# Performance work log

Hardware: AMD Instinct MI355X
Metric: run time of the kernel (lower is better)

Reference implementation:

```python
import jax, jax.numpy as jnp
import numpy as np

D = 256      # d_model
H = 8        # n_heads
L = 4        # n_levels
P = 4        # n_points
DFF = 1024   # d_ffn
DH = D // H  # head dim
SPATIAL = np.array([[100, 100], [50, 50], [25, 25], [13, 13]], dtype=np.int64)  # (H_l, W_l)
LV = int((SPATIAL[:, 0] * SPATIAL[:, 1]).sum())  # 13294 flattened memory tokens


def layer_norm(x, w, b, eps=1e-5):
    m = jnp.mean(x, -1, keepdims=True)
    v = jnp.mean((x - m) ** 2, -1, keepdims=True)
    return (x - m) * jax.lax.rsqrt(v + eps) * w + b


def setup_inputs() -> dict:
    key = jax.random.key(0)
    ks = jax.random.split(key, 16)
    nq, bs = 900, 8

    def w(k, shape, s=0.02):
        return jax.random.normal(k, shape, dtype=jnp.float32) * s

    return {
        "tgt": jax.random.normal(ks[0], (nq, bs, D), jnp.float32),
        "tgt_query_pos": jax.random.normal(ks[1], (nq, bs, D), jnp.float32),
        "tgt_reference_points": jax.random.uniform(ks[2], (nq, bs, L, 2), jnp.float32),
        "memory": jax.random.normal(ks[3], (LV, bs, D), jnp.float32),
        "sa_Wqkv": w(ks[4], (3 * D, D)), "sa_bqkv": jnp.zeros((3 * D,), jnp.float32),
        "sa_Wo": w(ks[5], (D, D)), "sa_bo": jnp.zeros((D,), jnp.float32),
        "ln1_w": jnp.ones((D,), jnp.float32), "ln1_b": jnp.zeros((D,), jnp.float32),
        "ln2_w": jnp.ones((D,), jnp.float32), "ln2_b": jnp.zeros((D,), jnp.float32),
        "ln3_w": jnp.ones((D,), jnp.float32), "ln3_b": jnp.zeros((D,), jnp.float32),
        "ca_Woff": w(ks[6], (H * L * P * 2, D)), "ca_boff": w(ks[7], (H * L * P * 2,), 0.5),
        "ca_Wattn": w(ks[8], (H * L * P, D)), "ca_battn": jnp.zeros((H * L * P,), jnp.float32),
        "ca_Wval": w(ks[9], (D, D)), "ca_bval": jnp.zeros((D,), jnp.float32),
        "ca_Wout": w(ks[10], (D, D)), "ca_bout": jnp.zeros((D,), jnp.float32),
        "ffn_W1": w(ks[11], (DFF, D)), "ffn_b1": jnp.zeros((DFF,), jnp.float32),
        "ffn_W2": w(ks[12], (D, DFF)), "ffn_b2": jnp.zeros((D,), jnp.float32),
        "memory_key_padding_mask": jnp.zeros((bs, LV), jnp.bool_),
        "memory_spatial_shapes": jnp.asarray(SPATIAL),
    }


def msdeform_attn(query, ref, value, mask, shapes_np,
                  Woff, boff, Wattn, battn, Wval, bval, Wout, bout):
    # query: [bs,nq,D], ref: [bs,nq,L,2], value: [bs,lv,D], mask: [bs,lv]
    bs, nq, _ = query.shape
    lv = value.shape[1]
    v = value @ Wval.T + bval
    v = jnp.where(mask[:, :, None], 0.0, v)
    v = v.reshape(bs, lv, H, DH).transpose(0, 2, 1, 3)  # [bs,H,lv,DH]
    off = (query @ Woff.T + boff).reshape(bs, nq, H, L, P, 2)
    aw = jax.nn.softmax((query @ Wattn.T + battn).reshape(bs, nq, H, L * P), -1)
    aw = aw.reshape(bs, nq, H, L, P)
    # offset normalizer is [W_l, H_l]
    norm = jnp.asarray(shapes_np[:, ::-1].copy(), jnp.float32)  # [L,2]
    loc = ref[:, :, None, :, None, :] + off / norm[None, None, None, :, None, :]
    out = jnp.zeros((bs, nq, H, DH), jnp.float32)
    start = 0
    for l in range(L):
        Hl, Wl = int(shapes_np[l, 0]), int(shapes_np[l, 1])
        vf = v[:, :, start:start + Hl * Wl]  # [bs,H,Hl*Wl,DH]
        start += Hl * Wl
        # grid_sample(align_corners=False) pixel coords
        x = loc[:, :, :, l, :, 0] * Wl - 0.5  # [bs,nq,H,P]
        y = loc[:, :, :, l, :, 1] * Hl - 0.5
        x0 = jnp.floor(x); y0 = jnp.floor(y)
        fx = x - x0; fy = y - y0
        x0i = x0.astype(jnp.int32); y0i = y0.astype(jnp.int32)

        def gather(yi, xi):
            valid = ((xi >= 0) & (xi < Wl) & (yi >= 0) & (yi < Hl)).astype(jnp.float32)
            idx = jnp.clip(yi, 0, Hl - 1) * Wl + jnp.clip(xi, 0, Wl - 1)
            idx_t = idx.transpose(0, 2, 1, 3).reshape(bs, H, nq * P, 1)
            g = jnp.take_along_axis(vf, idx_t, axis=2)  # [bs,H,nq*P,DH]
            return g * valid.transpose(0, 2, 1, 3).reshape(bs, H, nq * P, 1)

        def wgt(w):
            return w.transpose(0, 2, 1, 3).reshape(bs, H, nq * P, 1)

        samp = (gather(y0i, x0i) * wgt((1 - fx) * (1 - fy))
                + gather(y0i, x0i + 1) * wgt(fx * (1 - fy))
                + gather(y0i + 1, x0i) * wgt((1 - fx) * fy)
                + gather(y0i + 1, x0i + 1) * wgt(fx * fy))
        samp = samp.reshape(bs, H, nq, P, DH)
        out = out + jnp.einsum('bhqpd,bqhp->bqhd', samp, aw[:, :, :, l])
    return out.reshape(bs, nq, D) @ Wout.T + bout


def reference(tgt, tgt_query_pos, tgt_reference_points, memory,
              sa_Wqkv, sa_bqkv, sa_Wo, sa_bo,
              ln1_w, ln1_b, ln2_w, ln2_b, ln3_w, ln3_b,
              ca_Woff, ca_boff, ca_Wattn, ca_battn, ca_Wval, ca_bval, ca_Wout, ca_bout,
              ffn_W1, ffn_b1, ffn_W2, ffn_b2,
              memory_key_padding_mask, memory_spatial_shapes):
    shapes_np = np.asarray(memory_spatial_shapes)  # static per trace
    nq, bs, _ = tgt.shape
    # --- self attention (post-LN, residual) ---
    q = tgt + tgt_query_pos
    qp = (q @ sa_Wqkv[:D].T + sa_bqkv[:D]).reshape(nq, bs, H, DH)
    kp = (q @ sa_Wqkv[D:2 * D].T + sa_bqkv[D:2 * D]).reshape(nq, bs, H, DH)
    vp = (tgt @ sa_Wqkv[2 * D:].T + sa_bqkv[2 * D:]).reshape(nq, bs, H, DH)
    scores = jnp.einsum('qbhd,kbhd->bhqk', qp, kp) * (1.0 / float(np.sqrt(DH)))
    attn = jax.nn.softmax(scores, -1)
    o = jnp.einsum('bhqk,kbhd->qbhd', attn, vp).reshape(nq, bs, D) @ sa_Wo.T + sa_bo
    tgt = layer_norm(tgt + o, ln2_w, ln2_b)
    # --- multi-scale deformable cross attention ---
    query = (tgt + tgt_query_pos).transpose(1, 0, 2)      # [bs,nq,D]
    ref = tgt_reference_points.transpose(1, 0, 2, 3)      # [bs,nq,L,2]
    val = memory.transpose(1, 0, 2)                       # [bs,lv,D]
    ca = msdeform_attn(query, ref, val, memory_key_padding_mask, shapes_np,
                       ca_Woff, ca_boff, ca_Wattn, ca_battn,
                       ca_Wval, ca_bval, ca_Wout, ca_bout).transpose(1, 0, 2)
    tgt = layer_norm(tgt + ca, ln1_w, ln1_b)
    # --- FFN ---
    t2 = jax.nn.relu(tgt @ ffn_W1.T + ffn_b1) @ ffn_W2.T + ffn_b2
    return layer_norm(tgt + t2, ln3_w, ln3_b)
```

## Files before the change

### kernel.cpp

```cpp
#include <hip/hip_runtime.h>
#include <hip/hip_bf16.h>

#define NQ   900
#define BSZ  8
#define DM   256
#define NH   8
#define DHD  32
#define DFF_ 1024
#define LVTOT 13294
#define NTOK (NQ*BSZ)
#define MVAL (LVTOT*BSZ)

typedef __attribute__((ext_vector_type(8))) short bf16x8;
typedef __attribute__((ext_vector_type(4))) short bf16x4;
typedef __attribute__((ext_vector_type(4))) float f32x4;
typedef unsigned int u32;

__device__ __forceinline__ unsigned short f2bf(float x) {
  union { __hip_bfloat16 h; unsigned short u; } cv;
  cv.h = __float2bfloat16(x);
  return cv.u;
}
__device__ __forceinline__ float bf2f(unsigned short u) {
  union { __hip_bfloat16 h; unsigned short u; } cv;
  cv.u = u;
  return __bfloat162float(cv.h);
}

__device__ __forceinline__ void gl_lds16(const void* gsrc, void* ldst) {
  __builtin_amdgcn_global_load_lds(
      (const __attribute__((address_space(1))) u32*)gsrc,
      (__attribute__((address_space(3))) u32*)ldst, 16, 0, 0);
}

__global__ __launch_bounds__(256) void cast_kernel(const float* __restrict__ src,
                                                   unsigned short* __restrict__ dst, int n8) {
  int i = blockIdx.x * 256 + threadIdx.x;
  if (i >= n8) return;
  float4 a = ((const float4*)src)[i * 2];
  float4 b = ((const float4*)src)[i * 2 + 1];
  bf16x8 v;
  v[0] = (short)f2bf(a.x); v[1] = (short)f2bf(a.y);
  v[2] = (short)f2bf(a.z); v[3] = (short)f2bf(a.w);
  v[4] = (short)f2bf(b.x); v[5] = (short)f2bf(b.y);
  v[6] = (short)f2bf(b.z); v[7] = (short)f2bf(b.w);
  *(bf16x8*)(dst + (long)i * 8) = v;
}

__global__ __launch_bounds__(256) void addcast_kernel(const float* __restrict__ a,
                                                      const float* __restrict__ b,
                                                      unsigned short* __restrict__ o, int n8) {
  int i = blockIdx.x * 256 + threadIdx.x;
  if (i >= n8) return;
  float4 a0 = ((const float4*)a)[i * 2], a1 = ((const float4*)a)[i * 2 + 1];
  float4 b0 = ((const float4*)b)[i * 2], b1 = ((const float4*)b)[i * 2 + 1];
  bf16x8 v;
  v[0] = (short)f2bf(a0.x + b0.x); v[1] = (short)f2bf(a0.y + b0.y);
  v[2] = (short)f2bf(a0.z + b0.z); v[3] = (short)f2bf(a0.w + b0.w);
  v[4] = (short)f2bf(a1.x + b1.x); v[5] = (short)f2bf(a1.y + b1.y);
  v[6] = (short)f2bf(a1.z + b1.z); v[7] = (short)f2bf(a1.w + b1.w);
  *(bf16x8*)(o + (long)i * 8) = v;
}

__global__ __launch_bounds__(256) void cast_weights_kernel(
    const float* p0, const float* p1, const float* p2, const float* p3,
    const float* p4, const float* p5, const float* p6, const float* p7,
    unsigned short* dst) {
  long i8 = ((long)blockIdx.x * 256 + threadIdx.x) * 8;
  if (i8 >= 1015808) return;
  const float* src; long off;
  if      (i8 < 196608) { src = p0; off = i8; }
  else if (i8 < 262144) { src = p1; off = i8 - 196608; }
  else if (i8 < 327680) { src = p2; off = i8 - 262144; }
  else if (i8 < 393216) { src = p3; off = i8 - 327680; }
  else if (i8 < 425984) { src = p4; off = i8 - 393216; }
  else if (i8 < 491520) { src = p5; off = i8 - 425984; }
  else if (i8 < 753664) { src = p6; off = i8 - 491520; }
  else                  { src = p7; off = i8 - 753664; }
  float4 a = *(const float4*)(src + off);
  float4 b = *(const float4*)(src + off + 4);
  bf16x8 v;
  v[0] = (short)f2bf(a.x); v[1] = (short)f2bf(a.y);
  v[2] = (short)f2bf(a.z); v[3] = (short)f2bf(a.w);
  v[4] = (short)f2bf(b.x); v[5] = (short)f2bf(b.y);
  v[6] = (short)f2bf(b.z); v[7] = (short)f2bf(b.w);
  *(bf16x8*)(dst + i8) = v;
}

template <int AF32, int OUT_BF16, int RELU>
__global__ __launch_bounds__(256) void gemm_mfma_kernel(
    const void* __restrict__ Araw, const unsigned short* __restrict__ W,
    const float* __restrict__ bias, void* __restrict__ C,
    int M, int K, int ldc) {
  __shared__ unsigned short As[128 * 32];
  __shared__ unsigned short Bs[128 * 32];
  int tid = threadIdx.x;
  int l = tid & 63, w = tid >> 6;
  int lr = l & 15, lg = l >> 4;
  int wr = w >> 1, wc = w & 1;
  int n0 = blockIdx.x * 128, m0 = blockIdx.y * 128;

  f32x4 acc[4][4];
#pragma unroll
  for (int m = 0; m < 4; m++)
#pragma unroll
    for (int n = 0; n < 4; n++) acc[m][n] = (f32x4){0.f, 0.f, 0.f, 0.f};

  int srow = (l >> 2);
  int scol = (l & 3) * 8;

  for (int k0 = 0; k0 < K; k0 += 32) {
    if (k0) __syncthreads();
    if (AF32) {
      const float* Af = (const float*)Araw;
      int row = tid >> 1, c16 = (tid & 1) * 16;
      int arow = m0 + row; if (arow >= M) arow = M - 1;
      const float* ap = Af + (long)arow * K + k0 + c16;
      float4 f0 = *(const float4*)(ap + 0);
      float4 f1 = *(const float4*)(ap + 4);
      float4 f2 = *(const float4*)(ap + 8);
      float4 f3 = *(const float4*)(ap + 12);
      bf16x8 v0, v1;
      v0[0] = (short)f2bf(f0.x); v0[1] = (short)f2bf(f0.y);
      v0[2] = (short)f2bf(f0.z); v0[3] = (short)f2bf(f0.w);
      v0[4] = (short)f2bf(f1.x); v0[5] = (short)f2bf(f1.y);
      v0[6] = (short)f2bf(f1.z); v0[7] = (short)f2bf(f1.w);
      v1[0] = (short)f2bf(f2.x); v1[1] = (short)f2bf(f2.y);
      v1[2] = (short)f2bf(f2.z); v1[3] = (short)f2bf(f2.w);
      v1[4] = (short)f2bf(f3.x); v1[5] = (short)f2bf(f3.y);
      v1[6] = (short)f2bf(f3.z); v1[7] = (short)f2bf(f3.w);
      *(bf16x8*)&As[row * 32 + c16] = v0;
      *(bf16x8*)&As[row * 32 + c16 + 8] = v1;
      int browi = w * 16 + srow;
#pragma unroll
      for (int c = 0; c < 2; c++) {
        int row2 = c * 64 + browi;
        gl_lds16(W + (long)(n0 + row2) * K + k0 + scol, (char*)Bs + row2 * 64 + scol * 2);
      }
    } else {
      const unsigned short* A = (const unsigned short*)Araw;
#pragma unroll
      for (int c = 0; c < 2; c++) {
        int row = c * 64 + w * 16 + srow;
        if (m0 + c * 64 + w * 16 < M)
          gl_lds16(A + (long)(m0 + row) * K + k0 + scol, (char*)As + row * 64 + scol * 2);
        gl_lds16(W + (long)(n0 + row) * K + k0 + scol, (char*)Bs + row * 64 + scol * 2);
      }
    }
    __syncthreads();
    bf16x8 af[4], bf[4];
#pragma unroll
    for (int m = 0; m < 4; m++)
      af[m] = *(const bf16x8*)&As[(wr * 64 + m * 16 + lr) * 32 + lg * 8];
#pragma unroll
    for (int n = 0; n < 4; n++)
      bf[n] = *(const bf16x8*)&Bs[(wc * 64 + n * 16 + lr) * 32 + lg * 8];
#pragma unroll
    for (int m = 0; m < 4; m++)
#pragma unroll
      for (int n = 0; n < 4; n++)
        acc[m][n] = __builtin_amdgcn_mfma_f32_16x16x32_bf16(af[m], bf[n], acc[m][n], 0, 0, 0);
  }

  float bv[4];
#pragma unroll
  for (int ni = 0; ni < 4; ni++) bv[ni] = bias[n0 + wc * 64 + ni * 16 + lr];
#pragma unroll
  for (int mi = 0; mi < 4; mi++) {
#pragma unroll
    for (int r = 0; r < 4; r++) {
      int row = m0 + wr * 64 + mi * 16 + lg * 4 + r;
      if (row < M) {
#pragma unroll
        for (int ni = 0; ni < 4; ni++) {
          int col = n0 + wc * 64 + ni * 16 + lr;
          float v = acc[mi][ni][r] + bv[ni];
          if (RELU) v = fmaxf(v, 0.f);
          if (OUT_BF16) ((unsigned short*)C)[(long)row * ldc + col] = f2bf(v);
          else          ((float*)C)[(long)row * ldc + col] = v;
        }
      }
    }
  }
}

__global__ __launch_bounds__(256) void attn_mfma_kernel(const unsigned short* __restrict__ qkv,
                                                        unsigned short* __restrict__ out) {
  __shared__ unsigned short Vt[32][72];
  __shared__ unsigned short Ps[4][16][72];
  int tid = threadIdx.x;
  int l = tid & 63, w = tid >> 6;
  int lr = l & 15, lg = l >> 4;
  int q0 = blockIdx.x * 64;
  int h = blockIdx.y & 7, b = blockIdx.y >> 3;
  const float scale = 0.17677669529663687f;

  int qrow = q0 + w * 16 + lr;
  int qclamp = qrow < 899 ? qrow : 899;
  bf16x8 qf = *(const bf16x8*)(qkv + ((long)qclamp * 8 + b) * 768 + h * 32 + lg * 8);

  f32x4 o_acc[2];
  o_acc[0] = (f32x4){0.f, 0.f, 0.f, 0.f};
  o_acc[1] = (f32x4){0.f, 0.f, 0.f, 0.f};
  float m_run[4] = {-1e30f, -1e30f, -1e30f, -1e30f};
  float l_run[4] = {0.f, 0.f, 0.f, 0.f};

  for (int k0 = 0; k0 < NQ; k0 += 64) {
    __syncthreads();
    {
      int key = tid >> 2, dg = tid & 3;
      int kk = k0 + key; if (kk > 899) kk = 899;
      bf16x8 vv = *(const bf16x8*)(qkv + ((long)kk * 8 + b) * 768 + 512 + h * 32 + dg * 8);
#pragma unroll
      for (int j = 0; j < 8; j++) Vt[dg * 8 + j][key] = (unsigned short)vv[j];
    }
    f32x4 sg[4];
#pragma unroll
    for (int ng = 0; ng < 4; ng++) {
      int key = k0 + ng * 16 + lr; int kc = key < 899 ? key : 899;
      bf16x8 kf = *(const bf16x8*)(qkv + ((long)kc * 8 + b) * 768 + 256 + h * 32 + lg * 8);
      sg[ng] = __builtin_amdgcn_mfma_f32_16x16x32_bf16(qf, kf, (f32x4){0.f, 0.f, 0.f, 0.f}, 0, 0, 0);
    }
    float sv[4][4];
#pragma unroll
    for (int ng = 0; ng < 4; ng++) {
      bool bad = (k0 + ng * 16 + lr) >= NQ;
#pragma unroll
      for (int r = 0; r < 4; r++) sv[ng][r] = bad ? -1e30f : sg[ng][r] * scale;
    }
    float p[4][4];
#pragma unroll
    for (int r = 0; r < 4; r++) {
      float rmax = fmaxf(fmaxf(sv[0][r], sv[1][r]), fmaxf(sv[2][r], sv[3][r]));
#pragma unroll
      for (int mk = 8; mk; mk >>= 1) rmax = fmaxf(rmax, __shfl_xor(rmax, mk));
      float mnew = fmaxf(m_run[r], rmax);
      float fs = __expf(m_run[r] - mnew);
      m_run[r] = mnew;
      float ps = 0.f;
#pragma unroll
      for (int ng = 0; ng < 4; ng++) { p[ng][r] = __expf(sv[ng][r] - mnew); ps += p[ng][r]; }
#pragma unroll
      for (int mk = 8; mk; mk >>= 1) ps += __shfl_xor(ps, mk);
      l_run[r] = l_run[r] * fs + ps;
      o_acc[0][r] *= fs;
      o_acc[1][r] *= fs;
    }
#pragma unroll
    for (int ng = 0; ng < 4; ng++)
#pragma unroll
      for (int r = 0; r < 4; r++)
        Ps[w][lg * 4 + r][lr + ng * 16] = f2bf(p[ng][r]);
    __syncthreads();
#pragma unroll
    for (int ks = 0; ks < 2; ks++) {
      bf16x8 pf = *(const bf16x8*)&Ps[w][lr][ks * 32 + lg * 8];
#pragma unroll
      for (int ni = 0; ni < 2; ni++) {
        bf16x8 vf = *(const bf16x8*)&Vt[ni * 16 + lr][ks * 32 + lg * 8];
        o_acc[ni] = __builtin_amdgcn_mfma_f32_16x16x32_bf16(pf, vf, o_acc[ni], 0, 0, 0);
      }
    }
  }
#pragma unroll
  for (int r = 0; r < 4; r++) {
    int orow = q0 + w * 16 + lg * 4 + r;
    if (orow < NQ) {
      float inv = 1.f / l_run[r];
      unsigned short* op = out + ((long)orow * 8 + b) * 256 + h * 32 + lr;
      op[0]  = f2bf(o_acc[0][r] * inv);
      op[16] = f2bf(o_acc[1][r] * inv);
    }
  }
}

__device__ __forceinline__ void fetch4_acc(const unsigned short* __restrict__ vtmp, int lo, int W,
                                           int yi, int xi, int b, int col0, float wgt,
                                           float& a0, float& a1, float& a2, float& a3) {
  bool valid = (xi >= 0) & (xi < W) & (yi >= 0) & (yi < W);
  if (!valid) return;
  const unsigned short* p = vtmp + ((long)((lo + yi * W + xi) * BSZ + b)) * 256 + col0;
  bf16x4 r = *(const bf16x4*)p;
  a0 += wgt * bf2f((unsigned short)r[0]);
  a1 += wgt * bf2f((unsigned short)r[1]);
  a2 += wgt * bf2f((unsigned short)r[2]);
  a3 += wgt * bf2f((unsigned short)r[3]);
}

__global__ __launch_bounds__(256) void sampler_kernel(const unsigned short* __restrict__ vtmp,
                                                      const float* __restrict__ off,
                                                      const float* __restrict__ logits,
                                                      const float* __restrict__ ref,
                                                      unsigned short* __restrict__ samp) {
  __shared__ float s_off[4][256];
  __shared__ float s_aw[4][128];
  __shared__ float s_ref[4][8];
  int tid = threadIdx.x;
  int t0 = blockIdx.x * 4;
#pragma unroll
  for (int k = 0; k < 4; k++) s_off[k][tid] = off[(long)(t0 + k) * 256 + tid];
  if (tid < 128) {
#pragma unroll
    for (int k = 0; k < 4; k++) s_aw[k][tid] = logits[(long)(t0 + k) * 128 + tid];
  }
  if (tid < 32) s_ref[tid >> 3][tid & 7] = ref[(long)(t0 + (tid >> 3)) * 8 + (tid & 7)];
  __syncthreads();
  if (tid < 32) {
    int k = tid >> 3, hh = tid & 7;
    float* p = &s_aw[k][hh * 16];
    float m = -1e30f;
#pragma unroll
    for (int j = 0; j < 16; j++) m = fmaxf(m, p[j]);
    float s = 0.f;
#pragma unroll
    for (int j = 0; j < 16; j++) { p[j] = __expf(p[j] - m); s += p[j]; }
    float inv = 1.f / s;
#pragma unroll
    for (int j = 0; j < 16; j++) p[j] *= inv;
  }
  __syncthreads();
  int w = tid >> 6, l = tid & 63;
  int t = t0 + w;
  int h = l >> 3, col0 = h * 32 + (l & 7) * 4;
  int b = t & 7;
  const int Wls[4]  = {100, 50, 25, 13};
  const int lofs[4] = {0, 10000, 12500, 13125};
  float a0 = 0.f, a1 = 0.f, a2 = 0.f, a3 = 0.f;
#pragma unroll
  for (int lvl = 0; lvl < 4; lvl++) {
    int W = Wls[lvl];
    float Wf = (float)W;
    int lo = lofs[lvl];
    float rx = s_ref[w][lvl * 2 + 0], ry = s_ref[w][lvl * 2 + 1];
#pragma unroll
    for (int p = 0; p < 4; p++) {
      float ox = s_off[w][((h * 4 + lvl) * 4 + p) * 2 + 0];
      float oy = s_off[w][((h * 4 + lvl) * 4 + p) * 2 + 1];
      float x = rx * Wf + ox - 0.5f;
      float y = ry * Wf + oy - 0.5f;
      float x0f = floorf(x), y0f = floorf(y);
      float fx = x - x0f, fy = y - y0f;
      int x0 = (int)x0f, y0 = (int)y0f;
      float aa = s_aw[w][h * 16 + lvl * 4 + p];
      float w00 = aa * (1.f - fx) * (1.f - fy);
      float w01 = aa * fx * (1.f - fy);
      float w10 = aa * (1.f - fx) * fy;
      float w11 = aa * fx * fy;
      fetch4_acc(vtmp, lo, W, y0,     x0,     b, col0, w00, a0, a1, a2, a3);
      fetch4_acc(vtmp, lo, W, y0,     x0 + 1, b, col0, w01, a0, a1, a2, a3);
      fetch4_acc(vtmp, lo, W, y0 + 1, x0,     b, col0, w10, a0, a1, a2, a3);
      fetch4_acc(vtmp, lo, W, y0 + 1, x0 + 1, b, col0, w11, a0, a1, a2, a3);
    }
  }
  bf16x4 o;
  o[0] = (short)f2bf(a0); o[1] = (short)f2bf(a1);
  o[2] = (short)f2bf(a2); o[3] = (short)f2bf(a3);
  *(bf16x4*)(samp + (long)t * 256 + col0) = o;
}

__global__ __launch_bounds__(256) void ln_kernel(const float* __restrict__ x,
                                                 const float* __restrict__ res,
                                                 const float* __restrict__ w,
                                                 const float* __restrict__ bvec,
                                                 float* __restrict__ out,
                                                 unsigned short* __restrict__ out_bf,
                                                 const float* __restrict__ pos,
                                                 unsigned short* __restrict__ pos_bf,
                                                 int rows) {
  int wv = threadIdx.x >> 6, lane = threadIdx.x & 63;
  int row = blockIdx.x * 4 + wv;
  if (row >= rows) return;
  float4 xv = *(const float4*)(x + (long)row * 256 + lane * 4);
  float4 rv = *(const float4*)(res + (long)row * 256 + lane * 4);
  float v0 = xv.x + rv.x, v1 = xv.y + rv.y, v2 = xv.z + rv.z, v3 = xv.w + rv.w;
  float s = v0 + v1 + v2 + v3;
#pragma unroll
  for (int o = 32; o; o >>= 1) s += __shfl_xor(s, o);
  float mean = s * (1.f / 256.f);
  float d0 = v0 - mean, d1 = v1 - mean, d2 = v2 - mean, d3 = v3 - mean;
  float q = d0 * d0 + d1 * d1 + d2 * d2 + d3 * d3;
#pragma unroll
  for (int o = 32; o; o >>= 1) q += __shfl_xor(q, o);
  float rstd = rsqrtf(q * (1.f / 256.f) + 1e-5f);
  float4 wv4 = *(const float4*)(w + lane * 4);
  float4 bv4 = *(const float4*)(bvec + lane * 4);
  float o0 = d0 * rstd * wv4.x + bv4.x;
  float o1 = d1 * rstd * wv4.y + bv4.y;
  float o2 = d2 * rstd * wv4.z + bv4.z;
  float o3 = d3 * rstd * wv4.w + bv4.w;
  *(float4*)(out + (long)row * 256 + lane * 4) = make_float4(o0, o1, o2, o3);
  if (out_bf) {
    unsigned short* p = out_bf + (long)row * 256 + lane * 4;
    p[0] = f2bf(o0); p[1] = f2bf(o1); p[2] = f2bf(o2); p[3] = f2bf(o3);
  }
  if (pos_bf) {
    float4 pv = *(const float4*)(pos + (long)row * 256 + lane * 4);
    unsigned short* p = pos_bf + (long)row * 256 + lane * 4;
    p[0] = f2bf(o0 + pv.x); p[1] = f2bf(o1 + pv.y);
    p[2] = f2bf(o2 + pv.z); p[3] = f2bf(o3 + pv.w);
  }
}

extern "C" void kernel_launch(void* const* d_in, const int* in_sizes, int n_in,
                              void* d_out, int out_size, void* d_ws, size_t ws_size,
                              hipStream_t stream) {
  const float* tgt     = (const float*)d_in[0];
  const float* pos     = (const float*)d_in[1];
  const float* refpts  = (const float*)d_in[2];
  const float* memory  = (const float*)d_in[3];
  const float* sa_Wqkv = (const float*)d_in[4];
  const float* sa_bqkv = (const float*)d_in[5];
  const float* sa_Wo   = (const float*)d_in[6];
  const float* sa_bo   = (const float*)d_in[7];
  const float* ln1_w   = (const float*)d_in[8];
  const float* ln1_b   = (const float*)d_in[9];
  const float* ln2_w   = (const float*)d_in[10];
  const float* ln2_b   = (const float*)d_in[11];
  const float* ln3_w   = (const float*)d_in[12];
  const float* ln3_b   = (const float*)d_in[13];
  const float* ca_Woff = (const float*)d_in[14];
  const float* ca_boff = (const float*)d_in[15];
  const float* ca_Wattn= (const float*)d_in[16];
  const float* ca_battn= (const float*)d_in[17];
  const float* ca_Wval = (const float*)d_in[18];
  const float* ca_bval = (const float*)d_in[19];
  const float* ca_Wout = (const float*)d_in[20];
  const float* ca_bout = (const float*)d_in[21];
  const float* ffn_W1  = (const float*)d_in[22];
  const float* ffn_b1  = (const float*)d_in[23];
  const float* ffn_W2  = (const float*)d_in[24];
  const float* ffn_b2  = (const float*)d_in[25];

  char* ws = (char*)d_ws;
  float*          buf_ca = (float*)(ws);
  float*          buf_t3 = (float*)(ws + 8388608);
  unsigned short* t3_bf  = (unsigned short*)(ws + 16777216);
  unsigned short* buf_h  = (unsigned short*)(ws + 20971520);
  float*          buf_f  = (float*)(ws + 36700160);
  unsigned short* buf_v  = (unsigned short*)(ws + 54452224);
  unsigned short* wts    = (unsigned short*)(ws + 112590848);
  unsigned short* buf_q  = (unsigned short*)(ws + 114622464);
  unsigned short* buf_qkv= (unsigned short*)(ws + 118308864);
  float*          buf_off= (float*)(ws + 118308864);
  float*          buf_aw = (float*)(ws + 125681664);
  unsigned short* buf_o  = (unsigned short*)(ws + 129368064);
  unsigned short* buf_smp= (unsigned short*)(ws + 129368064);
  float*          buf_t2 = (float*)(ws + 133054464);

  const unsigned short* w_qkv = wts + 0;
  const unsigned short* w_o   = wts + 196608;
  const unsigned short* w_val = wts + 262144;
  const unsigned short* w_off = wts + 327680;
  const unsigned short* w_atn = wts + 393216;
  const unsigned short* w_out = wts + 425984;
  const unsigned short* w_f1  = wts + 491520;
  const unsigned short* w_f2  = wts + 753664;

  dim3 blk(256);
  const int n8tok = NTOK * DM / 8;

  cast_weights_kernel<<<(1015808 / 8 + 255) / 256, blk, 0, stream>>>(
      sa_Wqkv, sa_Wo, ca_Wval, ca_Woff, ca_Wattn, ca_Wout, ffn_W1, ffn_W2, wts);
  addcast_kernel<<<(n8tok + 255) / 256, blk, 0, stream>>>(tgt, pos, buf_q, n8tok);
  gemm_mfma_kernel<0, 1, 0><<<dim3(4, 57), blk, 0, stream>>>(buf_q, w_qkv, sa_bqkv,
                                                             buf_qkv, NTOK, 256, 768);
  gemm_mfma_kernel<1, 1, 0><<<dim3(2, 57), blk, 0, stream>>>(tgt, w_qkv + 512 * 256,
                                                             sa_bqkv + 512, buf_qkv + 512,
                                                             NTOK, 256, 768);
  gemm_mfma_kernel<1, 1, 0><<<dim3(2, 831), blk, 0, stream>>>(memory, w_val, ca_bval,
                                                              buf_v, MVAL, 256, 256);
  attn_mfma_kernel<<<dim3(15, 64), blk, 0, stream>>>(buf_qkv, buf_o);
  gemm_mfma_kernel<0, 0, 0><<<dim3(2, 57), blk, 0, stream>>>(buf_o, w_o, sa_bo,
                                                             buf_t2, NTOK, 256, 256);
  ln_kernel<<<1800, blk, 0, stream>>>(buf_t2, tgt, ln2_w, ln2_b, buf_t2, nullptr,
                                      pos, buf_q, NTOK);
  gemm_mfma_kernel<0, 0, 0><<<dim3(2, 57), blk, 0, stream>>>(buf_q, w_off, ca_boff,
                                                             buf_off, NTOK, 256, 256);
  gemm_mfma_kernel<0, 0, 0><<<dim3(1, 57), blk, 0, stream>>>(buf_q, w_atn, ca_battn,
                                                             buf_aw, NTOK, 256, 128);
  sampler_kernel<<<NTOK / 4, blk, 0, stream>>>(buf_v, buf_off, buf_aw, refpts, buf_smp);
  gemm_mfma_kernel<0, 0, 0><<<dim3(2, 57), blk, 0, stream>>>(buf_smp, w_out, ca_bout,
                                                             buf_ca, NTOK, 256, 256);
  ln_kernel<<<1800, blk, 0, stream>>>(buf_ca, buf_t2, ln1_w, ln1_b, buf_t3, t3_bf,
                                      nullptr, nullptr, NTOK);
  gemm_mfma_kernel<0, 1, 1><<<dim3(8, 57), blk, 0, stream>>>(t3_bf, w_f1, ffn_b1,
                                                             buf_h, NTOK, 256, 1024);
  gemm_mfma_kernel<0, 0, 0><<<dim3(2, 57), blk, 0, stream>>>(buf_h, w_f2, ffn_b2,
                                                             buf_f, NTOK, 1024, 256);
  ln_kernel<<<1800, blk, 0, stream>>>(buf_f, buf_t3, ln3_w, ln3_b, (float*)d_out, nullptr,
                                      nullptr, nullptr, NTOK);
}
```

Baseline: 250.1 us.

## Double-buffer GEMM LDS tiles with swizzled async loads, fp32 A staged directly

```diff
diff --git a/kernel.cpp b/kernel.cpp
--- a/kernel.cpp
+++ b/kernel.cpp
@@ -31,20 +31,6 @@
   __builtin_amdgcn_global_load_lds(
       (const __attribute__((address_space(1))) u32*)gsrc,
       (__attribute__((address_space(3))) u32*)ldst, 16, 0, 0);
-}
-
-__global__ __launch_bounds__(256) void cast_kernel(const float* __restrict__ src,
-                                                   unsigned short* __restrict__ dst, int n8) {
-  int i = blockIdx.x * 256 + threadIdx.x;
-  if (i >= n8) return;
-  float4 a = ((const float4*)src)[i * 2];
-  float4 b = ((const float4*)src)[i * 2 + 1];
-  bf16x8 v;
-  v[0] = (short)f2bf(a.x); v[1] = (short)f2bf(a.y);
-  v[2] = (short)f2bf(a.z); v[3] = (short)f2bf(a.w);
-  v[4] = (short)f2bf(b.x); v[5] = (short)f2bf(b.y);
-  v[6] = (short)f2bf(b.z); v[7] = (short)f2bf(b.w);
-  *(bf16x8*)(dst + (long)i * 8) = v;
 }
 
 __global__ __launch_bounds__(256) void addcast_kernel(const float* __restrict__ a,
@@ -92,8 +78,9 @@
     const void* __restrict__ Araw, const unsigned short* __restrict__ W,
     const float* __restrict__ bias, void* __restrict__ C,
     int M, int K, int ldc) {
-  __shared__ unsigned short As[128 * 32];
-  __shared__ unsigned short Bs[128 * 32];
+  constexpr int ABYTES = AF32 ? 16384 : 8192;
+  __shared__ alignas(16) unsigned char As[2][ABYTES];
+  __shared__ alignas(16) unsigned char Bs[2][8192];
   int tid = threadIdx.x;
   int l = tid & 63, w = tid >> 6;
   int lr = l & 15, lg = l >> 4;
@@ -106,60 +93,84 @@
 #pragma unroll
     for (int n = 0; n < 4; n++) acc[m][n] = (f32x4){0.f, 0.f, 0.f, 0.f};
 
-  int srow = (l >> 2);
-  int scol = (l & 3) * 8;
-
-  for (int k0 = 0; k0 < K; k0 += 32) {
-    if (k0) __syncthreads();
+  auto stageB = [&](int buf, int k0) {
+#pragma unroll
+    for (int i = 0; i < 2; i++) {
+      int c16 = i * 4 + w;
+      int row = c16 * 16 + (l >> 2);
+      int sc = (l & 3) ^ (row & 3);
+      gl_lds16(W + (long)(n0 + row) * K + k0 + sc * 8,
+               (unsigned char*)Bs[buf] + c16 * 1024 + l * 16);
+    }
+  };
+  auto stageA16 = [&](int buf, int k0) {
+    const unsigned short* A = (const unsigned short*)Araw;
+#pragma unroll
+    for (int i = 0; i < 2; i++) {
+      int c16 = i * 4 + w;
+      int row = c16 * 16 + (l >> 2);
+      int g = m0 + row; if (g >= M) g = M - 1;
+      int sc = (l & 3) ^ (row & 3);
+      gl_lds16(A + (long)g * K + k0 + sc * 8,
+               (unsigned char*)As[buf] + c16 * 1024 + l * 16);
+    }
+  };
+  auto stageA32 = [&](int buf, int k0) {
+    const float* Af = (const float*)Araw;
+#pragma unroll
+    for (int i = 0; i < 4; i++) {
+      int c8 = i * 4 + w;
+      int row = c8 * 8 + (l >> 3);
+      int g = m0 + row; if (g >= M) g = M - 1;
+      int sc = (l & 7) ^ (row & 7);
+      gl_lds16(Af + (long)g * K + k0 + sc * 4,
+               (unsigned char*)As[buf] + c8 * 1024 + l * 16);
+    }
+  };
+
+  int nt = K >> 5;
+  if (AF32) stageA32(0, 0); else stageA16(0, 0);
+  stageB(0, 0);
+
+  for (int t = 0; t < nt; t++) {
+    int buf = t & 1;
+    __syncthreads();
+    if (t + 1 < nt) {
+      int k1 = (t + 1) << 5;
+      if (AF32) stageA32(buf ^ 1, k1); else stageA16(buf ^ 1, k1);
+      stageB(buf ^ 1, k1);
+    }
+    bf16x8 af[4], bfr[4];
     if (AF32) {
-      const float* Af = (const float*)Araw;
-      int row = tid >> 1, c16 = (tid & 1) * 16;
-      int arow = m0 + row; if (arow >= M) arow = M - 1;
-      const float* ap = Af + (long)arow * K + k0 + c16;
-      float4 f0 = *(const float4*)(ap + 0);
-      float4 f1 = *(const float4*)(ap + 4);
-      float4 f2 = *(const float4*)(ap + 8);
-      float4 f3 = *(const float4*)(ap + 12);
-      bf16x8 v0, v1;
-      v0[0] = (short)f2bf(f0.x); v0[1] = (short)f2bf(f0.y);
-      v0[2] = (short)f2bf(f0.z); v0[3] = (short)f2bf(f0.w);
-      v0[4] = (short)f2bf(f1.x); v0[5] = (short)f2bf(f1.y);
-      v0[6] = (short)f2bf(f1.z); v0[7] = (short)f2bf(f1.w);
-      v1[0] = (short)f2bf(f2.x); v1[1] = (short)f2bf(f2.y);
-      v1[2] = (short)f2bf(f2.z); v1[3] = (short)f2bf(f2.w);
-      v1[4] = (short)f2bf(f3.x); v1[5] = (short)f2bf(f3.y);
-      v1[6] = (short)f2bf(f3.z); v1[7] = (short)f2bf(f3.w);
-      *(bf16x8*)&As[row * 32 + c16] = v0;
-      *(bf16x8*)&As[row * 32 + c16 + 8] = v1;
-      int browi = w * 16 + srow;
-#pragma unroll
-      for (int c = 0; c < 2; c++) {
-        int row2 = c * 64 + browi;
-        gl_lds16(W + (long)(n0 + row2) * K + k0 + scol, (char*)Bs + row2 * 64 + scol * 2);
+#pragma unroll
+      for (int m = 0; m < 4; m++) {
+        int row = wr * 64 + m * 16 + lr;
+        f32x4 fa = *(const f32x4*)(As[buf] + row * 128 + (((lg * 2)     ^ (lr & 7)) * 16));
+        f32x4 fb = *(const f32x4*)(As[buf] + row * 128 + (((lg * 2 + 1) ^ (lr & 7)) * 16));
+        bf16x8 v;
+        v[0] = (short)f2bf(fa[0]); v[1] = (short)f2bf(fa[1]);
+        v[2] = (short)f2bf(fa[2]); v[3] = (short)f2bf(fa[3]);
+        v[4] = (short)f2bf(fb[0]); v[5] = (short)f2bf(fb[1]);
+        v[6] = (short)f2bf(fb[2]); v[7] = (short)f2bf(fb[3]);
+        af[m] = v;
       }
     } else {
-      const unsigned short* A = (const unsigned short*)Araw;
-#pragma unroll
-      for (int c = 0; c < 2; c++) {
-        int row = c * 64 + w * 16 + srow;
-        if (m0 + c * 64 + w * 16 < M)
-          gl_lds16(A + (long)(m0 + row) * K + k0 + scol, (char*)As + row * 64 + scol * 2);
-        gl_lds16(W + (long)(n0 + row) * K + k0 + scol, (char*)Bs + row * 64 + scol * 2);
+#pragma unroll
+      for (int m = 0; m < 4; m++) {
+        int row = wr * 64 + m * 16 + lr;
+        af[m] = *(const bf16x8*)(As[buf] + row * 64 + ((lg ^ (lr & 3)) * 16));
       }
     }
-    __syncthreads();
-    bf16x8 af[4], bf[4];
+#pragma unroll
+    for (int n = 0; n < 4; n++) {
+      int row = wc * 64 + n * 16 + lr;
+      bfr[n] = *(const bf16x8*)(Bs[buf] + row * 64 + ((lg ^ (lr & 3)) * 16));
+    }
 #pragma unroll
     for (int m = 0; m < 4; m++)
-      af[m] = *(const bf16x8*)&As[(wr * 64 + m * 16 + lr) * 32 + lg * 8];
-#pragma unroll
-    for (int n = 0; n < 4; n++)
-      bf[n] = *(const bf16x8*)&Bs[(wc * 64 + n * 16 + lr) * 32 + lg * 8];
-#pragma unroll
-    for (int m = 0; m < 4; m++)
 #pragma unroll
       for (int n = 0; n < 4; n++)
-        acc[m][n] = __builtin_amdgcn_mfma_f32_16x16x32_bf16(af[m], bf[n], acc[m][n], 0, 0, 0);
+        acc[m][n] = __builtin_amdgcn_mfma_f32_16x16x32_bf16(af[m], bfr[n], acc[m][n], 0, 0, 0);
   }
 
   float bv[4];
```

New measurement: 257.0 us. 2.8% more time.
